# Kernel tuning notes

Hardware: AMD Instinct MI355X
Metric: run time of the kernel (lower is better)

The kernel has to match this reference:

```python
import jax, jax.numpy as jnp
import numpy as np

HEADS = 16
HEAD_DIMS = 64
EMB = HEADS * HEAD_DIMS  # 1024
B, L = 4, 2048


def setup_inputs() -> dict:
    key = jax.random.key(0)
    ks = jax.random.split(key, 12)
    s = 0.02
    return {
        "query": jax.random.normal(ks[0], (B, L, EMB), jnp.float32),
        "key": jax.random.normal(ks[1], (B, L, EMB), jnp.float32),
        "value": jax.random.normal(ks[2], (B, L, EMB), jnp.float32),
        "mask": jax.random.randint(ks[3], (B, 1, 1, L), 0, 2, jnp.int32),
        "Wq": s * jax.random.normal(ks[4], (HEAD_DIMS, HEAD_DIMS), jnp.float32),
        "bq": jnp.zeros((HEAD_DIMS,), jnp.float32),
        "Wk": s * jax.random.normal(ks[5], (HEAD_DIMS, HEAD_DIMS), jnp.float32),
        "bk": jnp.zeros((HEAD_DIMS,), jnp.float32),
        "Wv": s * jax.random.normal(ks[6], (HEAD_DIMS, HEAD_DIMS), jnp.float32),
        "bv": jnp.zeros((HEAD_DIMS,), jnp.float32),
        "Wfc": s * jax.random.normal(ks[7], (EMB, EMB), jnp.float32),
        "bfc": jnp.zeros((EMB,), jnp.float32),
    }


def reference(query, key, value, mask, Wq, bq, Wk, bk, Wv, bv, Wfc, bfc):
    Batch, q_len = query.shape[0], query.shape[1]
    k_len, v_len = key.shape[1], value.shape[1]
    # split heads: [B, L, H, D]
    q = query.reshape(Batch, q_len, HEADS, HEAD_DIMS)
    k = key.reshape(Batch, k_len, HEADS, HEAD_DIMS)
    v = value.reshape(Batch, v_len, HEADS, HEAD_DIMS)
    # per-head linear projections (torch Linear: x @ W.T + b)
    q = jnp.einsum("bqhd,ed->bqhe", q, Wq) + bq
    k = jnp.einsum("bkhd,ed->bkhe", k, Wk) + bk
    v = jnp.einsum("bvhd,ed->bvhe", v, Wv) + bv
    # scores [B, H, Q, K]
    scores = jnp.einsum("bqhd,bkhd->bhqk", q, k)
    scores = jnp.where(mask == 0, jnp.float32(-1e20), scores)
    # NOTE: original torch code uses `//` (floor division) by sqrt(head_dims)
    scores = jnp.floor(scores / jnp.sqrt(jnp.float32(HEAD_DIMS)))
    attn = jax.nn.softmax(scores, axis=-1)
    out = jnp.einsum("bhqv,bvhd->bqhd", attn, v).reshape(Batch, q_len, EMB)
    return out @ Wfc.T + bfc
```

## Files before the change

kernel.cpp:

```cpp
#include <hip/hip_runtime.h>
#include <math.h>

#define HEADS 16
#define EMB 1024
#define BATCH 4
#define SEQ 2048

#define TILE_B 12288L
#define BH_B   (64L * TILE_B)
#define MT_B   65536L

typedef __bf16 bf16_t;
typedef __bf16 bf16x4 __attribute__((ext_vector_type(4)));
typedef __bf16 bf16x8 __attribute__((ext_vector_type(8)));
typedef float f32x4 __attribute__((ext_vector_type(4)));
typedef float f32x16 __attribute__((ext_vector_type(16)));
typedef unsigned int u32x4 __attribute__((ext_vector_type(4)));

__device__ __forceinline__ f32x16 mfma32(bf16x8 a, bf16x8 b, f32x16 c) {
    return __builtin_amdgcn_mfma_f32_32x32x16_bf16(a, b, c, 0, 0, 0);
}

__device__ __forceinline__ unsigned cvtpk(float lo, float hi) {
    unsigned r;
    asm("v_cvt_pk_bf16_f32 %0, %1, %2" : "=v"(r) : "v"(lo), "v"(hi));
    return r;
}

__device__ __forceinline__ void plswap(unsigned &a, unsigned &b) {
    asm volatile("v_permlane32_swap_b32 %0, %1" : "+v"(a), "+v"(b));
}

__device__ __forceinline__ unsigned short bfbits(float x) {
    return __builtin_bit_cast(unsigned short, (bf16_t)x);
}

__device__ __forceinline__ void pack_p(const float* p, bf16x8& pa0, bf16x8& pa1) {
    unsigned w0 = cvtpk(p[0], p[1]),   w1 = cvtpk(p[2], p[3]);
    unsigned w2 = cvtpk(p[4], p[5]),   w3 = cvtpk(p[6], p[7]);
    plswap(w0, w2); plswap(w1, w3);
    unsigned w4 = cvtpk(p[8], p[9]),   w5 = cvtpk(p[10], p[11]);
    unsigned w6 = cvtpk(p[12], p[13]), w7 = cvtpk(p[14], p[15]);
    plswap(w4, w6); plswap(w5, w7);
    u32x4 ua = {w0, w1, w2, w3};
    u32x4 ub = {w4, w5, w6, w7};
    pa0 = __builtin_bit_cast(bf16x8, ua);
    pa1 = __builtin_bit_cast(bf16x8, ub);
}

__global__ void nmask_kernel(const int* __restrict__ mask, float* __restrict__ nmaskf) {
    const int b = blockIdx.x;
    const int t = threadIdx.x;
    int cnt = 0;
    #pragma unroll
    for (int i = 0; i < SEQ / 256; ++i)
        cnt += (mask[b * SEQ + t + i * 256] == 0);
    #pragma unroll
    for (int d = 1; d < 64; d <<= 1) cnt += __shfl_xor(cnt, d);
    __shared__ int red[4];
    if ((t & 63) == 0) red[t >> 6] = cnt;
    __syncthreads();
    if (t == 0) nmaskf[b] = (float)(red[0] + red[1] + red[2] + red[3]);
}

__global__ void wconv_kernel(const float* __restrict__ w, char* __restrict__ wf, int n_elems) {
    int i = (blockIdx.x * 256 + threadIdx.x) * 4;
    if (i < n_elems) {
        int n = i >> 10, k = i & 1023;
        float4 f = *(const float4*)(w + i);
        bf16x4 o;
        o[0] = (bf16_t)f.x; o[1] = (bf16_t)f.y; o[2] = (bf16_t)f.z; o[3] = (bf16_t)f.w;
        long byt = (long)(n >> 5) * MT_B + (long)(k >> 4) * 1024
                 + (long)((n & 31) + 32 * ((k >> 3) & 1)) * 16 + (k & 7) * 2;
        *(bf16x4*)(wf + byt) = o;
    }
}

__global__ __launch_bounds__(256) void proj_kernel(
    const float* __restrict__ xq, const float* __restrict__ xk, const float* __restrict__ xv,
    const float* __restrict__ Wq, const float* __restrict__ bq,
    const float* __restrict__ Wk, const float* __restrict__ bk,
    const float* __restrict__ Wv, const float* __restrict__ bv,
    const int* __restrict__ mask,
    bf16_t* __restrict__ qh, bf16_t* __restrict__ ql,
    char* __restrict__ kvf)
{
    __shared__ float Xs[64][68];
    __shared__ float Ws[64][68];

    const int t   = threadIdx.x;
    const int mat = blockIdx.y;
    const int bh  = blockIdx.x >> 5;
    const int l0  = (blockIdx.x & 31) * 64;
    const int b   = bh >> 4;
    const int hh  = bh & 15;

    const float* __restrict__ X    = (mat == 0) ? xq : (mat == 1) ? xk : xv;
    const float* __restrict__ W    = (mat == 0) ? Wq : (mat == 1) ? Wk : Wv;
    const float* __restrict__ bias = (mat == 0) ? bq : (mat == 1) ? bk : bv;

    #pragma unroll
    for (int i = 0; i < 4; ++i) {
        int c    = t + i * 256;
        int l    = c >> 4;
        int dblk = (c & 15) * 4;
        float4 xv4 = *(const float4*)(X + ((long)(b * SEQ + l0 + l)) * EMB + hh * 64 + dblk);
        Xs[dblk + 0][l] = xv4.x; Xs[dblk + 1][l] = xv4.y;
        Xs[dblk + 2][l] = xv4.z; Xs[dblk + 3][l] = xv4.w;
        float4 wv4 = *(const float4*)(W + l * 64 + dblk);
        Ws[dblk + 0][l] = wv4.x; Ws[dblk + 1][l] = wv4.y;
        Ws[dblk + 2][l] = wv4.z; Ws[dblk + 3][l] = wv4.w;
    }
    __syncthreads();

    const int mi = (t & 15) * 4;
    const int ei = (t >> 4) * 4;
    float acc[4][4];
    #pragma unroll
    for (int i = 0; i < 4; ++i)
        #pragma unroll
        for (int j = 0; j < 4; ++j) acc[i][j] = 0.f;

    #pragma unroll 8
    for (int d = 0; d < 64; ++d) {
        float4 a = *(const float4*)&Xs[d][mi];
        float4 w = *(const float4*)&Ws[d][ei];
        const float av[4] = {a.x, a.y, a.z, a.w};
        const float wv[4] = {w.x, w.y, w.z, w.w};
        #pragma unroll
        for (int i = 0; i < 4; ++i)
            #pragma unroll
            for (int j = 0; j < 4; ++j)
                acc[i][j] = fmaf(av[i], wv[j], acc[i][j]);
    }

    const float bb[4] = {bias[ei + 0], bias[ei + 1], bias[ei + 2], bias[ei + 3]};

    float zm[4];
    #pragma unroll
    for (int i = 0; i < 4; ++i)
        zm[i] = (mat == 0 || mask[b * SEQ + l0 + mi + i] != 0) ? 1.0f : 0.0f;

    if (mat == 0) {
        #pragma unroll
        for (int i = 0; i < 4; ++i) {
            long addr = ((long)(bh * SEQ + l0 + mi + i)) * 64 + ei;
            bf16x4 h4, l4;
            #pragma unroll
            for (int j = 0; j < 4; ++j) {
                float y = acc[i][j] + bb[j];
                bf16_t hi = (bf16_t)y;
                h4[j] = hi;
                l4[j] = (bf16_t)(y - (float)hi);
            }
            *(bf16x4*)(qh + addr) = h4;
            *(bf16x4*)(ql + addr) = l4;
        }
    } else if (mat == 1) {
        char* kvb = kvf + (long)bh * BH_B;
        #pragma unroll
        for (int i = 0; i < 4; ++i) {
            int l = l0 + mi + i;
            bf16x4 h4, l4;
            #pragma unroll
            for (int j = 0; j < 4; ++j) {
                float y = (acc[i][j] + bb[j]) * zm[i];
                bf16_t hi = (bf16_t)y;
                h4[j] = hi;
                l4[j] = (bf16_t)(y - (float)hi);
            }
            long byt = (long)(l >> 5) * TILE_B + (long)(ei >> 4) * 1024
                     + (long)((l & 31) + 32 * ((ei >> 3) & 1)) * 16 + (ei & 7) * 2;
            *(bf16x4*)(kvb + byt) = h4;
            *(bf16x4*)(kvb + byt + 4096) = l4;
        }
    } else {
        char* kvb = kvf + (long)bh * BH_B;
        #pragma unroll
        for (int i = 0; i < 4; ++i) {
            int l = l0 + mi + i;
            long tb = (long)(l >> 5) * TILE_B + 8192 + (l & 7) * 2;
            int c2  = (l & 31) >> 4;
            int hfk = (l >> 3) & 1;
            #pragma unroll
            for (int jj = 0; jj < 4; ++jj) {
                int d = ei + jj;
                float val = (acc[i][jj] + bb[jj]) * zm[i];
                long byt = tb + (long)(((d >> 5) << 1) + c2) * 1024
                         + (long)((d & 31) + 32 * hfk) * 16;
                *(unsigned short*)(kvb + byt) = bfbits(val);
            }
        }
    }
}

__global__ __launch_bounds__(256, 2) void attn_kernel(
    const bf16_t* __restrict__ qh, const bf16_t* __restrict__ ql,
    const char* __restrict__ kvf, const float* __restrict__ nmaskf,
    char* __restrict__ af)
{
    const int g   = blockIdx.x;
    const int xcd = g & 7;
    const int s8  = g >> 3;
    const int bh  = ((s8 >> 3) << 3) + xcd;
    const int qb  = s8 & 7;
    const int b   = bh >> 4;
    const int hh  = bh & 15;

    const int lane = threadIdx.x & 63;
    const int wave = threadIdx.x >> 6;
    const int col  = lane & 31;
    const int hf   = lane >> 5;

    const int q0 = qb * 256 + wave * 64;

    const long qoff0 = ((long)(bh * SEQ + q0 + col)) * 64 + hf * 8;
    const long qoff1 = qoff0 + 32 * 64;
    bf16x8 qfh0[4], qfl0[4], qfh1[4], qfl1[4];
    #pragma unroll
    for (int c = 0; c < 4; ++c) {
        qfh0[c] = *(const bf16x8*)(qh + qoff0 + 16 * c);
        qfl0[c] = *(const bf16x8*)(ql + qoff0 + 16 * c);
        qfh1[c] = *(const bf16x8*)(qh + qoff1 + 16 * c);
        qfl1[c] = *(const bf16x8*)(ql + qoff1 + 16 * c);
    }

    const float nmk = nmaskf[b];

    const char* __restrict__ kvb = kvf + (long)bh * BH_B + (long)lane * 16;

    f32x16 o00 = {}, o01 = {}, o10 = {}, o11 = {};
    float l0 = 0.f, l1 = 0.f;

    bf16x8 kfh[4], kfl[4];
    #pragma unroll
    for (int c = 0; c < 4; ++c) {
        kfh[c] = *(const bf16x8*)(kvb + c * 1024);
        kfl[c] = *(const bf16x8*)(kvb + 4096 + c * 1024);
    }

    #pragma unroll 1
    for (int kt = 0; kt < SEQ; kt += 32) {
        const long toff = (long)(kt >> 5) * TILE_B;
        bf16x8 v00 = *(const bf16x8*)(kvb + toff + 8192);
        bf16x8 v01 = *(const bf16x8*)(kvb + toff + 9216);
        bf16x8 v10 = *(const bf16x8*)(kvb + toff + 10240);
        bf16x8 v11 = *(const bf16x8*)(kvb + toff + 11264);

        f32x16 s0 = {}, s1 = {};
        __builtin_amdgcn_s_setprio(1);
        #pragma unroll
        for (int c = 0; c < 4; ++c) {
            s0 = mfma32(kfh[c], qfh0[c], s0);
            s1 = mfma32(kfh[c], qfh1[c], s1);
            s0 = mfma32(kfl[c], qfh0[c], s0);
            s1 = mfma32(kfl[c], qfh1[c], s1);
            s0 = mfma32(kfh[c], qfl0[c], s0);
            s1 = mfma32(kfh[c], qfl1[c], s1);
        }
        __builtin_amdgcn_s_setprio(0);

        #pragma unroll
        for (int c = 0; c < 4; ++c) {
            kfh[c] = *(const bf16x8*)(kvb + toff + TILE_B + c * 1024);
            kfl[c] = *(const bf16x8*)(kvb + toff + TILE_B + 4096 + c * 1024);
        }

        {
            float p[16];
            #pragma unroll
            for (int r = 0; r < 16; ++r) {
                float sv = floorf(s0[r] * 0.125f);
                p[r] = __expf(sv);
                l0 += p[r];
            }
            bf16x8 pa0, pa1;
            pack_p(p, pa0, pa1);
            __builtin_amdgcn_s_setprio(1);
            o00 = mfma32(pa0, v00, o00);
            o00 = mfma32(pa1, v01, o00);
            o01 = mfma32(pa0, v10, o01);
            o01 = mfma32(pa1, v11, o01);
            __builtin_amdgcn_s_setprio(0);
        }
        {
            float p[16];
            #pragma unroll
            for (int r = 0; r < 16; ++r) {
                float sv = floorf(s1[r] * 0.125f);
                p[r] = __expf(sv);
                l1 += p[r];
            }
            bf16x8 pa0, pa1;
            pack_p(p, pa0, pa1);
            __builtin_amdgcn_s_setprio(1);
            o10 = mfma32(pa0, v00, o10);
            o10 = mfma32(pa1, v01, o10);
            o11 = mfma32(pa0, v10, o11);
            o11 = mfma32(pa1, v11, o11);
            __builtin_amdgcn_s_setprio(0);
        }
    }

    const long mtb = ((long)(b * SEQ + q0) >> 5) * MT_B;
    const int  hfo = (col >> 3) & 1;
    const int  job = (col & 7) * 2;
    const int  cf0 = hh * 4 + (col >> 4);
    const int  cf1 = cf0 + 2;
    {
        float ltot = l0 + __shfl_xor(l0, 32) - nmk;
        float linv = 1.0f / ltot;
        #pragma unroll
        for (int r = 0; r < 16; ++r) {
            int row = (r & 3) + ((r >> 2) << 3) + 4 * hf;
            float li = __shfl(linv, row);
            long lb = mtb + (long)(row + 32 * hfo) * 16 + job;
            *(unsigned short*)(af + lb + (long)cf0 * 1024) = bfbits(o00[r] * li);
            *(unsigned short*)(af + lb + (long)cf1 * 1024) = bfbits(o01[r] * li);
        }
    }
    {
        float ltot = l1 + __shfl_xor(l1, 32) - nmk;
        float linv = 1.0f / ltot;
        #pragma unroll
        for (int r = 0; r < 16; ++r) {
            int row = (r & 3) + ((r >> 2) << 3) + 4 * hf;
            float li = __shfl(linv, row);
            long lb = mtb + MT_B + (long)(row + 32 * hfo) * 16 + job;
            *(unsigned short*)(af + lb + (long)cf0 * 1024) = bfbits(o10[r] * li);
            *(unsigned short*)(af + lb + (long)cf1 * 1024) = bfbits(o11[r] * li);
        }
    }
}

__global__ __launch_bounds__(256) void fc_kernel(
    const char* __restrict__ af, const char* __restrict__ wf,
    const float* __restrict__ bias, float* __restrict__ out)
{
    const int lane = threadIdx.x & 63;
    const int wave = threadIdx.x >> 6;
    const int col  = lane & 31;
    const int hf   = lane >> 5;
    const int wm   = wave & 1;
    const int wn   = wave >> 1;
    const int m0   = blockIdx.x * 128 + wm * 64;
    const int n0   = blockIdx.y * 128 + wn * 64;

    f32x16 acc[2][2] = {};
    const char* afb = af + (long)(m0 >> 5) * MT_B + (long)lane * 16;
    const char* wfb = wf + (long)(n0 >> 5) * MT_B + (long)lane * 16;

    #pragma unroll 2
    for (int k0 = 0; k0 < EMB; k0 += 16) {
        const long ko = (long)(k0 >> 4) * 1024;
        bf16x8 a0 = *(const bf16x8*)(afb + ko);
        bf16x8 a1 = *(const bf16x8*)(afb + MT_B + ko);
        bf16x8 b0 = *(const bf16x8*)(wfb + ko);
        bf16x8 b1 = *(const bf16x8*)(wfb + MT_B + ko);
        acc[0][0] = mfma32(a0, b0, acc[0][0]);
        acc[0][1] = mfma32(a0, b1, acc[0][1]);
        acc[1][0] = mfma32(a1, b0, acc[1][0]);
        acc[1][1] = mfma32(a1, b1, acc[1][1]);
    }

    const float b0v = bias[n0 + col];
    const float b1v = bias[n0 + 32 + col];
    #pragma unroll
    for (int mt = 0; mt < 2; ++mt) {
        #pragma unroll
        for (int r = 0; r < 16; ++r) {
            int mrow = m0 + mt * 32 + (r & 3) + ((r >> 2) << 3) + 4 * hf;
            out[(long)mrow * EMB + n0 + col]      = acc[mt][0][r] + b0v;
            out[(long)mrow * EMB + n0 + 32 + col] = acc[mt][1][r] + b1v;
        }
    }
}

extern "C" void kernel_launch(void* const* d_in, const int* in_sizes, int n_in,
                              void* d_out, int out_size, void* d_ws, size_t ws_size,
                              hipStream_t stream)
{
    const float* q    = (const float*)d_in[0];
    const float* k    = (const float*)d_in[1];
    const float* v    = (const float*)d_in[2];
    const int*   mask = (const int*)  d_in[3];
    const float* Wq   = (const float*)d_in[4];
    const float* bq   = (const float*)d_in[5];
    const float* Wk   = (const float*)d_in[6];
    const float* bk   = (const float*)d_in[7];
    const float* Wv   = (const float*)d_in[8];
    const float* bv   = (const float*)d_in[9];
    const float* Wfc  = (const float*)d_in[10];
    const float* bfc  = (const float*)d_in[11];
    float* out = (float*)d_out;

    const long NP = (long)BATCH * HEADS * SEQ * 64;
    bf16_t* qhp = (bf16_t*)d_ws;
    bf16_t* qlp = qhp + NP;
    char*   kvf = (char*)(qlp + NP);
    char*   afp = kvf + 64L * BH_B;
    char*   wfp = afp + (long)(BATCH * SEQ / 32) * MT_B;
    float*  nmf = (float*)(wfp + (long)(EMB / 32) * MT_B);

    nmask_kernel<<<BATCH, 256, 0, stream>>>(mask, nmf);
    wconv_kernel<<<(EMB * EMB / 4) / 256, 256, 0, stream>>>(Wfc, wfp, EMB * EMB);

    dim3 gP(2048, 3);
    proj_kernel<<<gP, 256, 0, stream>>>(q, k, v, Wq, bq, Wk, bk, Wv, bv, mask,
                                        qhp, qlp, kvf);

    attn_kernel<<<512, 256, 0, stream>>>(qhp, qlp, kvf, nmf, afp);

    dim3 gC(64, 8);
    fc_kernel<<<gC, 256, 0, stream>>>(afp, wfp, bfc, out);
}
```

Baseline: 223.4 us.

## Stage K/V tiles in LDS via double-buffered global_load_lds and fold scale into K

Instead of every wave reading each 12 KB K/V tile from global memory into registers, the four waves of a block now each copy one 3 KB slice straight into a double-buffered LDS tile with global_load_lds. All waves then read the shared tile from LDS, which cuts redundant global/L2 traffic by sharing each tile across the block. In exchange it adds a block barrier every iteration and swaps the register prefetch of the next K tile for LDS reads. Separately, the 1/8 score scale is folded into the K projection epilogue, removing one multiply per score element in the softmax loop.

```diff
diff --git a/kernel.cpp b/kernel.cpp
--- a/kernel.cpp
+++ b/kernel.cpp
@@ -33,6 +33,13 @@
 
 __device__ __forceinline__ unsigned short bfbits(float x) {
     return __builtin_bit_cast(unsigned short, (bf16_t)x);
+}
+
+__device__ __forceinline__ void gload_lds16(const void* g, void* l) {
+    __builtin_amdgcn_global_load_lds(
+        (const __attribute__((address_space(1))) void*)g,
+        (__attribute__((address_space(3))) void*)l,
+        16, 0, 0);
 }
 
 __device__ __forceinline__ void pack_p(const float* p, bf16x8& pa0, bf16x8& pa1) {
@@ -164,7 +171,7 @@
             bf16x4 h4, l4;
             #pragma unroll
             for (int j = 0; j < 4; ++j) {
-                float y = (acc[i][j] + bb[j]) * zm[i];
+                float y = (acc[i][j] + bb[j]) * zm[i] * 0.125f;
                 bf16_t hi = (bf16_t)y;
                 h4[j] = hi;
                 l4[j] = (bf16_t)(y - (float)hi);
@@ -199,6 +206,8 @@
     const char* __restrict__ kvf, const float* __restrict__ nmaskf,
     char* __restrict__ af)
 {
+    __shared__ __align__(16) char kvt[2][12288];
+
     const int g   = blockIdx.x;
     const int xcd = g & 7;
     const int s8  = g >> 3;
@@ -226,26 +235,44 @@
     }
 
     const float nmk = nmaskf[b];
-
-    const char* __restrict__ kvb = kvf + (long)bh * BH_B + (long)lane * 16;
+    const char* __restrict__ kvg = kvf + (long)bh * BH_B;
 
     f32x16 o00 = {}, o01 = {}, o10 = {}, o11 = {};
     float l0 = 0.f, l1 = 0.f;
 
-    bf16x8 kfh[4], kfl[4];
-    #pragma unroll
-    for (int c = 0; c < 4; ++c) {
-        kfh[c] = *(const bf16x8*)(kvb + c * 1024);
-        kfl[c] = *(const bf16x8*)(kvb + 4096 + c * 1024);
-    }
+    const int fbase = wave * 3 * 1024;
+
+    {
+        const char* src = kvg + fbase + (long)lane * 16;
+        #pragma unroll
+        for (int f = 0; f < 3; ++f)
+            gload_lds16(src + f * 1024, &kvt[0][fbase + f * 1024]);
+    }
+    __syncthreads();
 
     #pragma unroll 1
-    for (int kt = 0; kt < SEQ; kt += 32) {
-        const long toff = (long)(kt >> 5) * TILE_B;
-        bf16x8 v00 = *(const bf16x8*)(kvb + toff + 8192);
-        bf16x8 v01 = *(const bf16x8*)(kvb + toff + 9216);
-        bf16x8 v10 = *(const bf16x8*)(kvb + toff + 10240);
-        bf16x8 v11 = *(const bf16x8*)(kvb + toff + 11264);
+    for (int it = 0; it < 64; ++it) {
+        const int cur = it & 1;
+        const int nxt = (it < 63) ? it + 1 : 63;
+
+        {
+            const char* src = kvg + (long)nxt * TILE_B + fbase + (long)lane * 16;
+            #pragma unroll
+            for (int f = 0; f < 3; ++f)
+                gload_lds16(src + f * 1024, &kvt[cur ^ 1][fbase + f * 1024]);
+        }
+
+        const char* kb = &kvt[cur][0] + (long)lane * 16;
+        bf16x8 kfh[4], kfl[4];
+        #pragma unroll
+        for (int c = 0; c < 4; ++c) {
+            kfh[c] = *(const bf16x8*)(kb + c * 1024);
+            kfl[c] = *(const bf16x8*)(kb + 4096 + c * 1024);
+        }
+        bf16x8 v00 = *(const bf16x8*)(kb + 8192);
+        bf16x8 v01 = *(const bf16x8*)(kb + 9216);
+        bf16x8 v10 = *(const bf16x8*)(kb + 10240);
+        bf16x8 v11 = *(const bf16x8*)(kb + 11264);
 
         f32x16 s0 = {}, s1 = {};
         __builtin_amdgcn_s_setprio(1);
@@ -260,17 +287,11 @@
         }
         __builtin_amdgcn_s_setprio(0);
 
-        #pragma unroll
-        for (int c = 0; c < 4; ++c) {
-            kfh[c] = *(const bf16x8*)(kvb + toff + TILE_B + c * 1024);
-            kfl[c] = *(const bf16x8*)(kvb + toff + TILE_B + 4096 + c * 1024);
-        }
-
         {
             float p[16];
             #pragma unroll
             for (int r = 0; r < 16; ++r) {
-                float sv = floorf(s0[r] * 0.125f);
+                float sv = floorf(s0[r]);
                 p[r] = __expf(sv);
                 l0 += p[r];
             }
@@ -287,7 +308,7 @@
             float p[16];
             #pragma unroll
             for (int r = 0; r < 16; ++r) {
-                float sv = floorf(s1[r] * 0.125f);
+                float sv = floorf(s1[r]);
                 p[r] = __expf(sv);
                 l1 += p[r];
             }
@@ -300,6 +321,8 @@
             o11 = mfma32(pa1, v11, o11);
             __builtin_amdgcn_s_setprio(0);
         }
+
+        __syncthreads();
     }
 
     const long mtb = ((long)(b * SEQ + q0) >> 5) * MT_B;
```

Measured after the change: 213.2 us. 1.05x faster.
